# Optimization experiments

Measured on AMD Instinct MI355X. Metric: run time of the kernel, lower is better.

Reference implementation:

```python
import jax, jax.numpy as jnp
import numpy as np

NUM_GROUPS = 32
NUM_HEADS = 8
EPS = 1e-5


def setup_inputs() -> dict:
    key = jax.random.key(0)
    ks = jax.random.split(key, 3)
    C = 512
    x = jax.random.normal(ks[0], (4, C, 48, 48), dtype=jnp.float32)
    gamma = jnp.ones((C,), jnp.float32)
    beta = jnp.zeros((C,), jnp.float32)
    w_qkv = jax.random.normal(ks[1], (C, 3 * C), jnp.float32) * (1.0 / np.sqrt(C))
    b_qkv = jnp.zeros((3 * C,), jnp.float32)
    w_proj = jax.random.normal(ks[2], (C, C), jnp.float32) * (1.0 / np.sqrt(C))
    b_proj = jnp.zeros((C,), jnp.float32)
    return {"x": x, "gamma": gamma, "beta": beta, "w_qkv": w_qkv,
            "b_qkv": b_qkv, "w_proj": w_proj, "b_proj": b_proj}


def group_norm(x, gamma, beta):
    # x: (b, c, h, w); 32 groups over channel dim
    b, c, h, w = x.shape
    xg = x.reshape(b, NUM_GROUPS, c // NUM_GROUPS, h, w)
    mu = jnp.mean(xg, axis=(2, 3, 4), keepdims=True)
    var = jnp.var(xg, axis=(2, 3, 4), keepdims=True)
    xn = ((xg - mu) * jax.lax.rsqrt(var + EPS)).reshape(b, c, h, w)
    return xn * gamma[None, :, None, None] + beta[None, :, None, None]


def reference(x, gamma, beta, w_qkv, b_qkv, w_proj, b_proj):
    b, c, h, w = x.shape
    hd = c // NUM_HEADS
    scale = hd ** -0.5
    xn = group_norm(x, gamma, beta)
    x_flat = xn.reshape(b, c, h * w).transpose(0, 2, 1)          # (b, s, c)
    qkv = x_flat @ w_qkv + b_qkv                                  # (b, s, 3c)
    q, k, v = jnp.split(qkv, 3, axis=-1)
    s = h * w
    # (b, heads, s, hd)
    q = q.reshape(b, s, NUM_HEADS, hd).transpose(0, 2, 1, 3)
    k = k.reshape(b, s, NUM_HEADS, hd).transpose(0, 2, 1, 3)
    v = v.reshape(b, s, NUM_HEADS, hd).transpose(0, 2, 1, 3)
    attn = jnp.einsum('bhqd,bhkd->bhqk', q, k) * scale            # (b, h, s, s)
    attn = jax.nn.softmax(attn, axis=-1)
    out = jnp.einsum('bhqk,bhkd->bhqd', attn, v)                  # (b, h, s, hd)
    out = out.transpose(0, 2, 1, 3).reshape(b, s, c)
    out = out @ w_proj + b_proj                                   # (b, s, c)
    return x + out.transpose(0, 2, 1).reshape(b, c, h, w)
```

## Files before the change

kernel.cpp:

```cpp
#include <hip/hip_runtime.h>
#include <hip/hip_bf16.h>
#include <stdint.h>

#define S_LEN 2304
#define C_DIM 512
#define NH 8
#define HD 64

typedef __attribute__((ext_vector_type(8))) __bf16 bf16x8;
typedef __attribute__((ext_vector_type(4))) float f32x4;
typedef __attribute__((ext_vector_type(16))) float f32x16;
typedef __attribute__((ext_vector_type(8))) unsigned short u16x8;
typedef __attribute__((ext_vector_type(4))) unsigned short u16x4;
typedef __attribute__((ext_vector_type(4))) unsigned int u32x4;

__device__ __forceinline__ unsigned short bf16u(float f) {
  __hip_bfloat16 h = __float2bfloat16(f);
  return __builtin_bit_cast(unsigned short, h);
}

__device__ __forceinline__ void load_lds16(const void* g, void* l) {
  __builtin_amdgcn_global_load_lds(
      (const __attribute__((address_space(1))) void*)g,
      (__attribute__((address_space(3))) void*)l, 16, 0, 0);
}

__global__ __launch_bounds__(256) void gn_stats_kernel(const float* __restrict__ x,
                                                       float* __restrict__ stats) {
  const int bg = blockIdx.x;
  const float4* src = (const float4*)(x + (size_t)bg * 36864);
  float s = 0.f, s2 = 0.f;
#pragma unroll
  for (int i = 0; i < 36; ++i) {
    float4 v = src[i * 256 + threadIdx.x];
    s += v.x + v.y + v.z + v.w;
    s2 += v.x * v.x + v.y * v.y + v.z * v.z + v.w * v.w;
  }
#pragma unroll
  for (int off = 1; off < 64; off <<= 1) {
    s += __shfl_xor(s, off);
    s2 += __shfl_xor(s2, off);
  }
  __shared__ float red[8];
  const int wid = threadIdx.x >> 6;
  if ((threadIdx.x & 63) == 0) { red[wid] = s; red[wid + 4] = s2; }
  __syncthreads();
  if (threadIdx.x == 0) {
    float S = red[0] + red[1] + red[2] + red[3];
    float S2 = red[4] + red[5] + red[6] + red[7];
    float mu = S * (1.f / 36864.f);
    float var = S2 * (1.f / 36864.f) - mu * mu;
    stats[bg * 2] = mu;
    stats[bg * 2 + 1] = rsqrtf(var + 1e-5f);
  }
}

__global__ __launch_bounds__(256) void gn_norm_t_kernel(
    const float* __restrict__ x, const float* __restrict__ gamma,
    const float* __restrict__ beta, const float* __restrict__ stats,
    unsigned short* __restrict__ xn) {
  __shared__ float tile[64][68];
  const int s0 = blockIdx.x * 64, c0 = blockIdx.y * 64, b = blockIdx.z;
  const int tid = threadIdx.x;
  {
    const int cl = tid >> 2, sc = (tid & 3) * 16;
    const float* src = x + ((size_t)b * C_DIM + c0 + cl) * S_LEN + s0 + sc;
#pragma unroll
    for (int i = 0; i < 4; ++i)
      *(float4*)&tile[cl][sc + i * 4] = *(const float4*)(src + i * 4);
  }
  __syncthreads();
  const int sl = tid >> 2, cc = (tid & 3) * 16;
  const int g = (c0 + cc) >> 4;
  const float mu = stats[((size_t)b * 32 + g) * 2];
  const float rs = stats[((size_t)b * 32 + g) * 2 + 1];
  u16x8 o0, o1;
#pragma unroll
  for (int j = 0; j < 8; ++j) {
    const int c = c0 + cc + j;
    o0[j] = bf16u((tile[cc + j][sl] - mu) * rs * gamma[c] + beta[c]);
  }
#pragma unroll
  for (int j = 0; j < 8; ++j) {
    const int c = c0 + cc + 8 + j;
    o1[j] = bf16u((tile[cc + 8 + j][sl] - mu) * rs * gamma[c] + beta[c]);
  }
  unsigned short* dst = xn + ((size_t)b * S_LEN + s0 + sl) * C_DIM + c0 + cc;
  *(u16x8*)dst = o0;
  *(u16x8*)(dst + 8) = o1;
}

__global__ __launch_bounds__(256) void wt_kernel(const float* __restrict__ w,
                                                 unsigned short* __restrict__ wT,
                                                 int N, int K) {
  __shared__ float tile[64][68];
  const int n0 = blockIdx.x * 64, k0 = blockIdx.y * 64;
  const int tid = threadIdx.x;
  {
    const int kl = tid >> 2, nc = (tid & 3) * 16;
    const float* src = w + (size_t)(k0 + kl) * N + n0 + nc;
#pragma unroll
    for (int i = 0; i < 4; ++i)
      *(float4*)&tile[kl][nc + i * 4] = *(const float4*)(src + i * 4);
  }
  __syncthreads();
  const int nl = tid >> 2, kc = (tid & 3) * 16;
  u16x8 o0, o1;
#pragma unroll
  for (int j = 0; j < 8; ++j) o0[j] = bf16u(tile[kc + j][nl]);
#pragma unroll
  for (int j = 0; j < 8; ++j) o1[j] = bf16u(tile[kc + 8 + j][nl]);
  unsigned short* dst = wT + (size_t)(n0 + nl) * K + k0 + kc;
  *(u16x8*)dst = o0;
  *(u16x8*)(dst + 8) = o1;
}

__device__ __forceinline__ void gemm128_core(const unsigned short* __restrict__ A,
                                             const unsigned short* __restrict__ B,
                                             int K, int m0, int n0, short* lds_a,
                                             short* lds_b, f32x4 (&acc)[4][4]) {
  const int tid = threadIdx.x;
  const int lane = tid & 63, wid = tid >> 6;
  const int wr = wid >> 1, wc = wid & 1;
  const f32x4 fzero = {0.f, 0.f, 0.f, 0.f};
#pragma unroll
  for (int i = 0; i < 4; ++i)
#pragma unroll
    for (int j = 0; j < 4; ++j) acc[i][j] = fzero;
  const int lrow = lane >> 3;
  const int lcol = (lane & 7) * 8;
  for (int kt = 0; kt < K; kt += 64) {
#pragma unroll
    for (int i = 0; i < 4; ++i) {
      const int r0 = (wid * 4 + i) * 8;
      load_lds16((const void*)(A + (size_t)(m0 + r0 + lrow) * K + kt + lcol), lds_a + r0 * 64);
      load_lds16((const void*)(B + (size_t)(n0 + r0 + lrow) * K + kt + lcol), lds_b + r0 * 64);
    }
    __syncthreads();
#pragma unroll
    for (int ks = 0; ks < 2; ++ks) {
      bf16x8 af[4], bfr[4];
#pragma unroll
      for (int mf = 0; mf < 4; ++mf)
        af[mf] = *(const bf16x8*)(lds_a + ((wr * 64 + mf * 16 + (lane & 15)) * 64 +
                                           ks * 32 + (lane >> 4) * 8));
#pragma unroll
      for (int nf = 0; nf < 4; ++nf)
        bfr[nf] = *(const bf16x8*)(lds_b + ((wc * 64 + nf * 16 + (lane & 15)) * 64 +
                                            ks * 32 + (lane >> 4) * 8));
#pragma unroll
      for (int mf = 0; mf < 4; ++mf)
#pragma unroll
        for (int nf = 0; nf < 4; ++nf)
          acc[mf][nf] =
              __builtin_amdgcn_mfma_f32_16x16x32_bf16(af[mf], bfr[nf], acc[mf][nf], 0, 0, 0);
    }
    __syncthreads();
  }
}

__global__ __launch_bounds__(256) void qkv_gemm_kernel(
    const unsigned short* __restrict__ xn, const unsigned short* __restrict__ wT,
    const float* __restrict__ bq, unsigned short* __restrict__ Qb,
    unsigned short* __restrict__ Kb, unsigned short* __restrict__ Vt) {
  __shared__ short lds_a[128 * 64];
  __shared__ short lds_b[128 * 64];
  const int b = blockIdx.z;
  const int m0 = blockIdx.x * 128, n0 = blockIdx.y * 128;
  f32x4 acc[4][4];
  gemm128_core(xn + (size_t)b * S_LEN * C_DIM, wT, C_DIM, m0, n0, lds_a, lds_b, acc);
  const int lane = threadIdx.x & 63, wid = threadIdx.x >> 6;
  const int wr = wid >> 1, wc = wid & 1;
#pragma unroll
  for (int mf = 0; mf < 4; ++mf) {
#pragma unroll
    for (int nf = 0; nf < 4; ++nf) {
      const int n = n0 + wc * 64 + nf * 16 + (lane & 15);
      const int part = n >> 9;
      const int h = (n >> 6) & 7;
      const int d = n & 63;
      const float bias = bq[n];
      const int m = m0 + wr * 64 + mf * 16 + (lane >> 4) * 4;
      if (part == 2) {
        u16x4 pk;
#pragma unroll
        for (int r = 0; r < 4; ++r) pk[r] = bf16u(acc[mf][nf][r] + bias);
        *(u16x4*)(Vt + ((size_t)(b * NH + h) * HD + d) * S_LEN + m) = pk;
      } else {
        unsigned short* dst = part == 0 ? Qb : Kb;
        const float sc = part == 0 ? 0.18033688011112042f : 1.0f;
#pragma unroll
        for (int r = 0; r < 4; ++r)
          dst[((size_t)(b * NH + h) * S_LEN + m + r) * HD + d] =
              bf16u((acc[mf][nf][r] + bias) * sc);
      }
    }
  }
}

#define QBLK 64
__global__ __launch_bounds__(256, 4) void attn_kernel(const unsigned short* __restrict__ Q,
                                                      const unsigned short* __restrict__ K,
                                                      const unsigned short* __restrict__ Vt,
                                                      unsigned short* __restrict__ O) {
  __shared__ __align__(16) char smem[32768];
  const int tid = threadIdx.x;
  const int w = tid >> 6, l = tid & 63;
  const int l31 = l & 31, hi = l >> 5;
  const int ks = w & 1, qw = w >> 1;
  const int L = blockIdx.y * 36 + blockIdx.x;
  const int xcd = L & 7, j = L >> 3;
  const int bh = xcd * 4 + j / 36;
  const int qt = j % 36;
  const int b = bh >> 3, h = bh & 7;
  const int q0 = qt * QBLK;

  const char* gQ = (const char*)Q + (size_t)bh * S_LEN * 128;
  const char* gK = (const char*)K + (size_t)bh * S_LEN * 128;
  const char* gV = (const char*)Vt + (size_t)bh * HD * (S_LEN * 2);

  bf16x8 qf[4];
  {
    const char* qp = gQ + (size_t)(q0 + qw * 32 + l31) * 128 + hi * 16;
#pragma unroll
    for (int d4 = 0; d4 < 4; ++d4) qf[d4] = *(const bf16x8*)(qp + d4 * 32);
  }

  const int sr = tid >> 3, sch = tid & 7;
  const char* pk0;
  const char* pv0;
  {
    pk0 = gK + (size_t)sr * 128 + ((sch ^ (sr & 7)) << 4);
    const int co = sch ^ (sr & 7);
    const int vd = 2 * sr + (co >> 2), slot = co & 3;
    pv0 = gV + (size_t)vd * (S_LEN * 2) + slot * 16;
  }
  const char* pk1 = pk0 + 1152 * 128;
  const char* pv1 = pv0 + 1152 * 2;

  auto stage = [&](int dbuf) {
    char* base = smem + dbuf * 8192 + tid * 16;
    load_lds16((const void*)pk0, base);
    load_lds16((const void*)pv0, base + 4096);
    load_lds16((const void*)pk1, base + 16384);
    load_lds16((const void*)pv1, base + 16384 + 4096);
    pk0 += 4096; pv0 += 64; pk1 += 4096; pv1 += 64;
  };

  stage(0);

  const u16x8 onesu = {0x3F80, 0x3F80, 0x3F80, 0x3F80, 0x3F80, 0x3F80, 0x3F80, 0x3F80};
  const bf16x8 onesf = __builtin_bit_cast(bf16x8, onesu);
  f32x16 z16;
#pragma unroll
  for (int i = 0; i < 16; ++i) z16[i] = 0.f;

  float m_run = -1e30f, lsum = 0.f;
  f32x16 oac0, oac1;
#pragma unroll
  for (int i = 0; i < 16; ++i) { oac0[i] = 0.f; oac1[i] = 0.f; }

  for (int kt = 0; kt < 36; ++kt) {
    if (kt < 35) {
      stage((kt + 1) & 1);
      asm volatile("s_waitcnt vmcnt(4)" ::: "memory");
    } else {
      asm volatile("s_waitcnt vmcnt(0)" ::: "memory");
    }
    __builtin_amdgcn_s_barrier();

    const char* kreg = smem + ks * 16384 + (kt & 1) * 8192;
    const char* vreg = kreg + 4096;

    f32x16 st;
#pragma unroll
    for (int i = 0; i < 16; ++i) st[i] = 0.f;
    {
      const int ksw = l31 & 7;
#pragma unroll
      for (int d4 = 0; d4 < 4; ++d4) {
        bf16x8 kf = *(const bf16x8*)(kreg + l31 * 128 + (((d4 * 2 + hi) ^ ksw) << 4));
        st = __builtin_amdgcn_mfma_f32_32x32x16_bf16(kf, qf[d4], st, 0, 0, 0);
      }
    }
    float t8[8];
#pragma unroll
    for (int i = 0; i < 8; ++i) t8[i] = fmaxf(st[2 * i], st[2 * i + 1]);
#pragma unroll
    for (int i = 0; i < 4; ++i) t8[i] = fmaxf(t8[i], t8[i + 4]);
    float mt = fmaxf(fmaxf(t8[0], t8[1]), fmaxf(t8[2], t8[3]));
    {
      float mo = mt;
      asm volatile("v_permlane32_swap_b32 %0, %1" : "+v"(mt), "+v"(mo));
      mt = fmaxf(mt, mo);
    }
    if (__any((mt - m_run) > 8.f)) {
      const float mnew = fmaxf(m_run, mt);
      const float corr = exp2f(m_run - mnew);
#pragma unroll
      for (int i = 0; i < 16; ++i) { oac0[i] *= corr; oac1[i] *= corr; }
      lsum *= corr;
      m_run = mnew;
    }
    float p[16];
#pragma unroll
    for (int i = 0; i < 16; ++i) p[i] = exp2f(st[i] - m_run);
    unsigned int wv[8];
#pragma unroll
    for (int jj = 0; jj < 8; ++jj)
      asm("v_cvt_pk_bf16_f32 %0, %1, %2" : "=v"(wv[jj]) : "v"(p[2 * jj]), "v"(p[2 * jj + 1]));
    asm volatile("v_permlane32_swap_b32 %0, %1" : "+v"(wv[0]), "+v"(wv[2]));
    asm volatile("v_permlane32_swap_b32 %0, %1" : "+v"(wv[1]), "+v"(wv[3]));
    asm volatile("v_permlane32_swap_b32 %0, %1" : "+v"(wv[4]), "+v"(wv[6]));
    asm volatile("v_permlane32_swap_b32 %0, %1" : "+v"(wv[5]), "+v"(wv[7]));
    u32x4 pw0 = {wv[0], wv[1], wv[2], wv[3]};
    u32x4 pw1 = {wv[4], wv[5], wv[6], wv[7]};
    bf16x8 pf0 = __builtin_bit_cast(bf16x8, pw0);
    bf16x8 pf1 = __builtin_bit_cast(bf16x8, pw1);
    {
      f32x16 tmp = __builtin_amdgcn_mfma_f32_32x32x16_bf16(onesf, pf0, z16, 0, 0, 0);
      tmp = __builtin_amdgcn_mfma_f32_32x32x16_bf16(onesf, pf1, tmp, 0, 0, 0);
      lsum += tmp[0];
    }
    {
      const int vr = l31 >> 1;
      const int c0 = ((l31 & 1) * 4 + hi) ^ (vr & 7);
      const int c1 = ((l31 & 1) * 4 + 2 + hi) ^ (vr & 7);
      bf16x8 vf0 = *(const bf16x8*)(vreg + vr * 128 + (c0 << 4));
      oac0 = __builtin_amdgcn_mfma_f32_32x32x16_bf16(vf0, pf0, oac0, 0, 0, 0);
      bf16x8 vf1 = *(const bf16x8*)(vreg + vr * 128 + (c1 << 4));
      oac0 = __builtin_amdgcn_mfma_f32_32x32x16_bf16(vf1, pf1, oac0, 0, 0, 0);
    }
    {
      const int vr = 16 + (l31 >> 1);
      const int c0 = ((l31 & 1) * 4 + hi) ^ (vr & 7);
      const int c1 = ((l31 & 1) * 4 + 2 + hi) ^ (vr & 7);
      bf16x8 vf0 = *(const bf16x8*)(vreg + vr * 128 + (c0 << 4));
      oac1 = __builtin_amdgcn_mfma_f32_32x32x16_bf16(vf0, pf0, oac1, 0, 0, 0);
      bf16x8 vf1 = *(const bf16x8*)(vreg + vr * 128 + (c1 << 4));
      oac1 = __builtin_amdgcn_mfma_f32_32x32x16_bf16(vf1, pf1, oac1, 0, 0, 0);
    }
    __builtin_amdgcn_s_barrier();
  }

  __syncthreads();
  float* fl = (float*)smem;
  float* obuf = fl + 512;
  if (hi == 0) {
    fl[w * 32 + l31] = m_run;
    fl[128 + w * 32 + l31] = lsum;
  }
  __syncthreads();
  const float pm = fl[(w ^ 1) * 32 + l31];
  const float pl = fl[128 + (w ^ 1) * 32 + l31];
  const float mM = fmaxf(m_run, pm);
  const float sOwn = exp2f(m_run - mM);
  const float newl = lsum * sOwn + pl * exp2f(pm - mM);
  const int q = qw * 32 + l31;
  if (ks == 0) {
    if (hi == 0) fl[256 + q] = 1.f / newl;
#pragma unroll
    for (int g = 0; g < 4; ++g) {
      float4 v0 = {oac0[g * 4] * sOwn, oac0[g * 4 + 1] * sOwn, oac0[g * 4 + 2] * sOwn,
                   oac0[g * 4 + 3] * sOwn};
      *(float4*)&obuf[q * 68 + g * 8 + hi * 4] = v0;
      float4 v1 = {oac1[g * 4] * sOwn, oac1[g * 4 + 1] * sOwn, oac1[g * 4 + 2] * sOwn,
                   oac1[g * 4 + 3] * sOwn};
      *(float4*)&obuf[q * 68 + 32 + g * 8 + hi * 4] = v1;
    }
  }
  __syncthreads();
  if (ks == 1) {
#pragma unroll
    for (int g = 0; g < 4; ++g) {
      float4 v0 = *(const float4*)&obuf[q * 68 + g * 8 + hi * 4];
      v0.x += oac0[g * 4] * sOwn; v0.y += oac0[g * 4 + 1] * sOwn;
      v0.z += oac0[g * 4 + 2] * sOwn; v0.w += oac0[g * 4 + 3] * sOwn;
      *(float4*)&obuf[q * 68 + g * 8 + hi * 4] = v0;
      float4 v1 = *(const float4*)&obuf[q * 68 + 32 + g * 8 + hi * 4];
      v1.x += oac1[g * 4] * sOwn; v1.y += oac1[g * 4 + 1] * sOwn;
      v1.z += oac1[g * 4 + 2] * sOwn; v1.w += oac1[g * 4 + 3] * sOwn;
      *(float4*)&obuf[q * 68 + 32 + g * 8 + hi * 4] = v1;
    }
  }
  __syncthreads();
#pragma unroll
  for (int i = 0; i < 2; ++i) {
    const int c = i * 256 + tid;
    const int r = c >> 3, ch = c & 7;
    const float invr = fl[256 + r];
    u16x8 o;
#pragma unroll
    for (int jj = 0; jj < 8; ++jj) o[jj] = bf16u(obuf[r * 68 + ch * 8 + jj] * invr);
    *(u16x8*)(O + ((size_t)b * S_LEN + q0 + r) * C_DIM + h * HD + ch * 8) = o;
  }
}

__global__ __launch_bounds__(256) void proj_gemm_kernel(
    const unsigned short* __restrict__ wT, const unsigned short* __restrict__ ao,
    const float* __restrict__ bp, const float* __restrict__ x, float* __restrict__ out) {
  __shared__ short lds_a[128 * 64];
  __shared__ short lds_b[128 * 64];
  const int b = blockIdx.z;
  const int m0 = blockIdx.x * 128, n0 = blockIdx.y * 128;
  f32x4 acc[4][4];
  gemm128_core(wT, ao + (size_t)b * S_LEN * C_DIM, C_DIM, m0, n0, lds_a, lds_b, acc);
  const int lane = threadIdx.x & 63, wid = threadIdx.x >> 6;
  const int wr = wid >> 1, wc = wid & 1;
#pragma unroll
  for (int mf = 0; mf < 4; ++mf) {
#pragma unroll
    for (int nf = 0; nf < 4; ++nf) {
      const int n = n0 + wc * 64 + nf * 16 + (lane & 15);
#pragma unroll
      for (int r = 0; r < 4; ++r) {
        const int m = m0 + wr * 64 + mf * 16 + (lane >> 4) * 4 + r;
        const size_t idx = ((size_t)b * C_DIM + m) * S_LEN + n;
        out[idx] = x[idx] + acc[mf][nf][r] + bp[m];
      }
    }
  }
}

extern "C" void kernel_launch(void* const* d_in, const int* in_sizes, int n_in,
                              void* d_out, int out_size, void* d_ws, size_t ws_size,
                              hipStream_t stream) {
  const float* x = (const float*)d_in[0];
  const float* gamma = (const float*)d_in[1];
  const float* beta = (const float*)d_in[2];
  const float* w_qkv = (const float*)d_in[3];
  const float* b_qkv = (const float*)d_in[4];
  const float* w_proj = (const float*)d_in[5];
  const float* b_proj = (const float*)d_in[6];
  float* out = (float*)d_out;

  char* ws = (char*)d_ws;
  float* stats = (float*)ws;
  unsigned short* xn = (unsigned short*)(ws + 1024);
  unsigned short* wqkvT = (unsigned short*)(ws + 9438208);
  unsigned short* wprojT = (unsigned short*)(ws + 11011072);
  unsigned short* Qb = (unsigned short*)(ws + 11535360);
  unsigned short* Kb = (unsigned short*)(ws + 20972544);
  unsigned short* Vt = (unsigned short*)(ws + 30409728);
  unsigned short* ao = (unsigned short*)(ws + 39846912);

  hipLaunchKernelGGL(gn_stats_kernel, dim3(128), dim3(256), 0, stream, x, stats);
  hipLaunchKernelGGL(wt_kernel, dim3(24, 8), dim3(256), 0, stream, w_qkv, wqkvT, 3 * C_DIM, C_DIM);
  hipLaunchKernelGGL(wt_kernel, dim3(8, 8), dim3(256), 0, stream, w_proj, wprojT, C_DIM, C_DIM);
  hipLaunchKernelGGL(gn_norm_t_kernel, dim3(36, 8, 4), dim3(256), 0, stream, x, gamma, beta, stats, xn);
  hipLaunchKernelGGL(qkv_gemm_kernel, dim3(18, 12, 4), dim3(256), 0, stream, xn, wqkvT, b_qkv, Qb, Kb, Vt);
  hipLaunchKernelGGL(attn_kernel, dim3(36, 32), dim3(256), 0, stream, Qb, Kb, Vt, ao);
  hipLaunchKernelGGL(proj_gemm_kernel, dim3(4, 18, 4), dim3(256), 0, stream, wprojT, ao, b_proj, x, out);
}
```

Baseline: 162.9 us.

## Restage attention K/V into MFMA fragment order and merge weight transposes

The attention kernel now has each lane copy global K/V into LDS at the exact spot it later reads its MFMA operand from. Inner-loop LDS reads become fixed offsets from one per-lane base instead of XOR-swizzled address arithmetic. The two weight-transpose launches are merged into one kernel that branches on blockIdx, saving a launch. Risks include LDS bank conflicts from the new layout, less coalesced global reads, and an extra wait and barrier after the first stage.

Measured after the change: 166.1 us (median of 2 runs). Within noise of the previous version (+2.0%).

```diff
diff --git a/kernel.cpp b/kernel.cpp
--- a/kernel.cpp
+++ b/kernel.cpp
@@ -90,11 +90,17 @@
   *(u16x8*)(dst + 8) = o1;
 }
 
-__global__ __launch_bounds__(256) void wt_kernel(const float* __restrict__ w,
-                                                 unsigned short* __restrict__ wT,
-                                                 int N, int K) {
+__global__ __launch_bounds__(256) void wt2_kernel(const float* __restrict__ w0,
+                                                  unsigned short* __restrict__ t0,
+                                                  const float* __restrict__ w1,
+                                                  unsigned short* __restrict__ t1) {
   __shared__ float tile[64][68];
-  const int n0 = blockIdx.x * 64, k0 = blockIdx.y * 64;
+  const float* w;
+  unsigned short* wT;
+  int N, n0;
+  if (blockIdx.x < 24) { w = w0; wT = t0; N = 1536; n0 = blockIdx.x * 64; }
+  else                 { w = w1; wT = t1; N = 512;  n0 = (blockIdx.x - 24) * 64; }
+  const int k0 = blockIdx.y * 64;
   const int tid = threadIdx.x;
   {
     const int kl = tid >> 2, nc = (tid & 3) * 16;
@@ -110,7 +116,7 @@
   for (int j = 0; j < 8; ++j) o0[j] = bf16u(tile[kc + j][nl]);
 #pragma unroll
   for (int j = 0; j < 8; ++j) o1[j] = bf16u(tile[kc + 8 + j][nl]);
-  unsigned short* dst = wT + (size_t)(n0 + nl) * K + k0 + kc;
+  unsigned short* dst = wT + (size_t)(n0 + nl) * 512 + k0 + kc;
   *(u16x8*)dst = o0;
   *(u16x8*)(dst + 8) = o1;
 }
@@ -226,15 +232,8 @@
     for (int d4 = 0; d4 < 4; ++d4) qf[d4] = *(const bf16x8*)(qp + d4 * 32);
   }
 
-  const int sr = tid >> 3, sch = tid & 7;
-  const char* pk0;
-  const char* pv0;
-  {
-    pk0 = gK + (size_t)sr * 128 + ((sch ^ (sr & 7)) << 4);
-    const int co = sch ^ (sr & 7);
-    const int vd = 2 * sr + (co >> 2), slot = co & 3;
-    pv0 = gV + (size_t)vd * (S_LEN * 2) + slot * 16;
-  }
+  const char* pk0 = gK + (size_t)l31 * 128 + ((w * 2 + hi) << 4);
+  const char* pv0 = gV + (size_t)((w >> 1) * 32 + l31) * (S_LEN * 2) + (((w & 1) * 2 + hi) << 4);
   const char* pk1 = pk0 + 1152 * 128;
   const char* pv1 = pv0 + 1152 * 2;
 
@@ -248,6 +247,8 @@
   };
 
   stage(0);
+  asm volatile("s_waitcnt vmcnt(0)" ::: "memory");
+  __builtin_amdgcn_s_barrier();
 
   const u16x8 onesu = {0x3F80, 0x3F80, 0x3F80, 0x3F80, 0x3F80, 0x3F80, 0x3F80, 0x3F80};
   const bf16x8 onesf = __builtin_bit_cast(bf16x8, onesu);
@@ -259,6 +260,8 @@
   f32x16 oac0, oac1;
 #pragma unroll
   for (int i = 0; i < 16; ++i) { oac0[i] = 0.f; oac1[i] = 0.f; }
+
+  const char* mybase = smem + ks * 16384 + l * 16;
 
   for (int kt = 0; kt < 36; ++kt) {
     if (kt < 35) {
@@ -269,19 +272,16 @@
     }
     __builtin_amdgcn_s_barrier();
 
-    const char* kreg = smem + ks * 16384 + (kt & 1) * 8192;
-    const char* vreg = kreg + 4096;
+    const char* kfb = mybase + (kt & 1) * 8192;
+    const char* vfb = kfb + 4096;
 
     f32x16 st;
 #pragma unroll
     for (int i = 0; i < 16; ++i) st[i] = 0.f;
-    {
-      const int ksw = l31 & 7;
-#pragma unroll
-      for (int d4 = 0; d4 < 4; ++d4) {
-        bf16x8 kf = *(const bf16x8*)(kreg + l31 * 128 + (((d4 * 2 + hi) ^ ksw) << 4));
-        st = __builtin_amdgcn_mfma_f32_32x32x16_bf16(kf, qf[d4], st, 0, 0, 0);
-      }
+#pragma unroll
+    for (int d4 = 0; d4 < 4; ++d4) {
+      bf16x8 kf = *(const bf16x8*)(kfb + d4 * 1024);
+      st = __builtin_amdgcn_mfma_f32_32x32x16_bf16(kf, qf[d4], st, 0, 0, 0);
     }
     float t8[8];
 #pragma unroll
@@ -323,21 +323,15 @@
       lsum += tmp[0];
     }
     {
-      const int vr = l31 >> 1;
-      const int c0 = ((l31 & 1) * 4 + hi) ^ (vr & 7);
-      const int c1 = ((l31 & 1) * 4 + 2 + hi) ^ (vr & 7);
-      bf16x8 vf0 = *(const bf16x8*)(vreg + vr * 128 + (c0 << 4));
+      bf16x8 vf0 = *(const bf16x8*)(vfb);
       oac0 = __builtin_amdgcn_mfma_f32_32x32x16_bf16(vf0, pf0, oac0, 0, 0, 0);
-      bf16x8 vf1 = *(const bf16x8*)(vreg + vr * 128 + (c1 << 4));
+      bf16x8 vf1 = *(const bf16x8*)(vfb + 1024);
       oac0 = __builtin_amdgcn_mfma_f32_32x32x16_bf16(vf1, pf1, oac0, 0, 0, 0);
     }
     {
-      const int vr = 16 + (l31 >> 1);
-      const int c0 = ((l31 & 1) * 4 + hi) ^ (vr & 7);
-      const int c1 = ((l31 & 1) * 4 + 2 + hi) ^ (vr & 7);
-      bf16x8 vf0 = *(const bf16x8*)(vreg + vr * 128 + (c0 << 4));
+      bf16x8 vf0 = *(const bf16x8*)(vfb + 2048);
       oac1 = __builtin_amdgcn_mfma_f32_32x32x16_bf16(vf0, pf0, oac1, 0, 0, 0);
-      bf16x8 vf1 = *(const bf16x8*)(vreg + vr * 128 + (c1 << 4));
+      bf16x8 vf1 = *(const bf16x8*)(vfb + 3072);
       oac1 = __builtin_amdgcn_mfma_f32_32x32x16_bf16(vf1, pf1, oac1, 0, 0, 0);
     }
     __builtin_amdgcn_s_barrier();
@@ -445,8 +439,7 @@
   unsigned short* ao = (unsigned short*)(ws + 39846912);
 
   hipLaunchKernelGGL(gn_stats_kernel, dim3(128), dim3(256), 0, stream, x, stats);
-  hipLaunchKernelGGL(wt_kernel, dim3(24, 8), dim3(256), 0, stream, w_qkv, wqkvT, 3 * C_DIM, C_DIM);
-  hipLaunchKernelGGL(wt_kernel, dim3(8, 8), dim3(256), 0, stream, w_proj, wprojT, C_DIM, C_DIM);
+  hipLaunchKernelGGL(wt2_kernel, dim3(32, 8), dim3(256), 0, stream, w_qkv, wqkvT, w_proj, wprojT);
   hipLaunchKernelGGL(gn_norm_t_kernel, dim3(36, 8, 4), dim3(256), 0, stream, x, gamma, beta, stats, xn);
   hipLaunchKernelGGL(qkv_gemm_kernel, dim3(18, 12, 4), dim3(256), 0, stream, xn, wqkvT, b_qkv, Qb, Kb, Vt);
   hipLaunchKernelGGL(attn_kernel, dim3(36, 32), dim3(256), 0, stream, Qb, Kb, Vt, ao);
```
